# Kernel optimization log

Hardware: AMD Instinct MI355X
Metric: run time of the kernel (lower is better)

Reference implementation:

```python
import jax, jax.numpy as jnp
import numpy as np

N = 150_000          # active BEV voxels
C = 128              # SHARED_CONV_CHANNEL
KK = 9               # 3x3 submanifold kernel
H = W = 1024         # BEV spatial shape at stride 8
OUT_CH = (3, 2, 1, 3, 2)   # hm, center, center_z, dim, rot
NH = 5
MAXO = 3
EPS = 1e-5
INIT_BIAS = -2.19


def _build_neighbor_idx():
    # Random sparse occupancy; pad index == N means 'inactive neighbor'
    rng = np.random.default_rng(0)
    flat = rng.choice(H * W, size=N, replace=False)
    ys, xs = flat // W, flat % W
    grid = np.full(H * W, N, dtype=np.int32)
    grid[flat] = np.arange(N, dtype=np.int32)
    nbr = np.full((N, KK), N, dtype=np.int32)
    k = 0
    for dy in (-1, 0, 1):
        for dx in (-1, 0, 1):
            ny, nx = ys + dy, xs + dx
            ok = (ny >= 0) & (ny < H) & (nx >= 0) & (nx < W)
            nbr[ok, k] = grid[(ny * W + nx)[ok]]
            k += 1
    return jnp.asarray(nbr)


def setup_inputs() -> dict:
    key = jax.random.key(0)
    k0, k1, k2 = jax.random.split(key, 3)
    x = jax.random.normal(k0, (N, C), jnp.float32)
    W1 = jax.random.normal(k1, (NH, KK, C, C), jnp.float32) * (2.0 / (KK * C)) ** 0.5  # kaiming
    gamma = jnp.ones((NH, C), jnp.float32)
    beta = jnp.zeros((NH, C), jnp.float32)
    W2 = jax.random.normal(k2, (NH, C, MAXO), jnp.float32) * 0.02
    b2 = jnp.zeros((NH, MAXO), jnp.float32).at[0, :OUT_CH[0]].set(INIT_BIAS)  # hm init_bias
    return {"x": x, "neighbor_idx": _build_neighbor_idx(),
            "W1": W1, "gamma": gamma, "beta": beta, "W2": W2, "b2": b2}


def reference(x, neighbor_idx, W1, gamma, beta, W2, b2):
    # pad row of zeros: inactive neighbors contribute nothing (submanifold conv)
    xp = jnp.concatenate([x, jnp.zeros((1, C), x.dtype)], axis=0)
    acc = jnp.zeros((NH, x.shape[0], C), x.dtype)
    for k in range(KK):                       # fixed 3x3 kernel loop
        g = xp[neighbor_idx[:, k]]            # [N, C] irregular gather
        acc = acc + jnp.einsum('nc,hcd->hnd', g, W1[:, k])
    # BatchNorm1d (training mode: batch stats over active voxels) + ReLU
    mean = acc.mean(axis=1, keepdims=True)
    var = ((acc - mean) ** 2).mean(axis=1, keepdims=True)
    h = (acc - mean) * jax.lax.rsqrt(var + EPS) * gamma[:, None, :] + beta[:, None, :]
    h = jax.nn.relu(h)
    # 1x1 SubMConv per head (padded to MAXO channels, masked)
    out = jnp.einsum('hnc,hco->hno', h, W2) + b2[:, None, :]   # [NH, N, MAXO]
    mask = (jnp.arange(MAXO)[None, :] < jnp.asarray(OUT_CH)[:, None]).astype(out.dtype)
    return out * mask[:, None, :]
```

## Files before the change

kernel.cpp:

```cpp
#include <hip/hip_runtime.h>

#define NPTS 150000
#define NHEAD 5
#define KTOT 1152
#define NTILES 1172
#define NBLK 586
#define HSTRIDE 592
#define EPSV 1e-5f

typedef __bf16 bf16x8 __attribute__((ext_vector_type(8)));
typedef float f32x4 __attribute__((ext_vector_type(4)));
typedef unsigned short u16x8 __attribute__((ext_vector_type(8)));

#define WS_NEEDED 238484416UL

__device__ __forceinline__ unsigned short f2bf(float f) {
    unsigned int u = __float_as_uint(f);
    u += 0x7FFFu + ((u >> 16) & 1u);
    return (unsigned short)(u >> 16);
}

__device__ __forceinline__ void gload16(const void* g, void* l) {
    __builtin_amdgcn_global_load_lds((const __attribute__((address_space(1))) void*)g,
                                     (__attribute__((address_space(3))) void*)l, 16, 0, 0);
}

__global__ void k_convert(const float* __restrict__ x, unsigned short* __restrict__ xbf) {
    const size_t i8 = (size_t)blockIdx.x * 256 + threadIdx.x;
    const size_t base = i8 * 8;
    if (base >= (size_t)(NPTS + 1) * 128) return;
    if (base < (size_t)NPTS * 128) {
        const f32x4 v0 = __builtin_nontemporal_load((const f32x4*)(x + base));
        const f32x4 v1 = __builtin_nontemporal_load((const f32x4*)(x + base + 4));
        u16x8 o;
        o[0] = f2bf(v0[0]); o[1] = f2bf(v0[1]); o[2] = f2bf(v0[2]); o[3] = f2bf(v0[3]);
        o[4] = f2bf(v1[0]); o[5] = f2bf(v1[1]); o[6] = f2bf(v1[2]); o[7] = f2bf(v1[3]);
        *(u16x8*)(xbf + base) = o;
    } else {
        u16x8 z = {0,0,0,0,0,0,0,0};
        *(u16x8*)(xbf + base) = z;
    }
}

__global__ void k_w1t(const float* __restrict__ W1, unsigned short* __restrict__ w1t) {
    const int idx = blockIdx.x * 256 + threadIdx.x;
    const int d = idx & 127;
    const int c = (idx >> 7) & 127;
    const int hk = idx >> 14;
    const int k = hk % 9, h = hk / 9;
    const int col = h * 128 + d;
    const int p = k * 128 + c;
    const int s32 = p >> 5;
    const int j0 = (p >> 3) & 3;
    const int jj = j0 ^ ((col >> 1) & 3);
    w1t[(size_t)col * KTOT + s32 * 32 + jj * 8 + (p & 7)] = f2bf(W1[idx]);
}

__global__ void k_hist(const int* __restrict__ nbr, int* __restrict__ hist_t) {
    __shared__ int lh[512];
    const int t = threadIdx.x, b = blockIdx.x;
    lh[t] = 0; lh[t + 256] = 0;
    __syncthreads();
    const int n = b * 256 + t;
    if (n < NPTS) {
        int pat = 0;
#pragma unroll
        for (int k = 0; k < 9; k++) pat |= (nbr[n * 9 + k] != NPTS) << k;
        atomicAdd(&lh[pat], 1);
    }
    __syncthreads();
    hist_t[t * HSTRIDE + b] = lh[t];
    hist_t[(t + 256) * HSTRIDE + b] = lh[t + 256];
}

__global__ void k_scan1(int* __restrict__ hist_t, int* __restrict__ tot) {
    const int p = blockIdx.x;
    const int lane = threadIdx.x;
    int run = 0;
    for (int c = 0; c < 10; c++) {
        const int i = c * 64 + lane;
        const int orig = (i < NBLK) ? hist_t[p * HSTRIDE + i] : 0;
        int v = orig;
        for (int d = 1; d < 64; d <<= 1) {
            const int w = __shfl_up(v, d);
            if (lane >= d) v += w;
        }
        if (i < NBLK) hist_t[p * HSTRIDE + i] = run + v - orig;
        run += __shfl(v, 63);
    }
    if (lane == 0) tot[p] = run;
}

__global__ void k_scan2(const int* __restrict__ tot, int* __restrict__ base) {
    __shared__ int t512[512];
    const int k = threadIdx.x;
    const int v = tot[k];
    t512[k] = v;
    __syncthreads();
    for (int d = 1; d < 512; d <<= 1) {
        const int w = (k >= d) ? t512[k - d] : 0;
        __syncthreads();
        t512[k] += w;
        __syncthreads();
    }
    base[k] = t512[k] - v;
}

__global__ void k_scatter(const int* __restrict__ nbr, const int* __restrict__ hist_t,
                          const int* __restrict__ base, int* __restrict__ perm) {
    __shared__ int pat_s[256];
    const int t = threadIdx.x, b = blockIdx.x;
    const int n = b * 256 + t;
    int pat = -1;
    if (n < NPTS) {
        pat = 0;
#pragma unroll
        for (int k = 0; k < 9; k++) pat |= (nbr[n * 9 + k] != NPTS) << k;
    }
    pat_s[t] = pat;
    __syncthreads();
    if (n < NPTS) {
        int rank = 0;
        for (int j = 0; j < 256; j++) rank += (j < t) & (pat_s[j] == pat);
        perm[base[pat] + hist_t[pat * HSTRIDE + b] + rank] = n;
    }
}

__global__ __launch_bounds__(512, 4) void k_gemm(
    const unsigned short* __restrict__ xbf,
    const unsigned short* __restrict__ w1t,
    const int* __restrict__ nbr,
    const int* __restrict__ perm,
    unsigned short* __restrict__ accw,
    float* __restrict__ partials)
{
    __shared__ unsigned short ABC[28672];
    __shared__ int nbr_s[9 * 128];
    __shared__ int perm_s[128];
    __shared__ int mask_s;

    const int tid = threadIdx.x;
    const int wid = tid >> 6;
    const int lane = tid & 63;
    const int bm = blockIdx.x;
    const int b2 = blockIdx.y;
    const int tile = (bm * 331) % NTILES;
    const int tile0 = tile * 128;

    if (tid == 0) mask_s = 0;
    if (tid < 128) {
        const int gr = tile0 + tid;
        perm_s[tid] = (gr < NPTS) ? perm[gr] : NPTS;
    }
    __syncthreads();
    if (tid < 128) {
        const int prow = perm_s[tid];
        int pat = 0;
#pragma unroll
        for (int k = 0; k < 9; k++) {
            const int v = (prow < NPTS) ? nbr[prow * 9 + k] : NPTS;
            nbr_s[k * 128 + tid] = v;
            pat |= (v != NPTS) << k;
        }
        if (pat) atomicOr(&mask_s, pat);
    }
    __syncthreads();
    const int mask = mask_s | 16;
    const int steps = 4 * __builtin_popcount(mask);

    const int RM = (wid >> 2) * 64;
    const int CNl = (wid & 3) * 80;
    const int lr16 = lane >> 2;
    const int lb = lane & 3;
    const int jswS = (lb ^ ((lr16 >> 1) & 3)) * 8;

    f32x4 acc[4][5];
#pragma unroll
    for (int m = 0; m < 4; m++)
#pragma unroll
        for (int n = 0; n < 5; n++) acc[m][n] = f32x4{0.f, 0.f, 0.f, 0.f};

    auto stage = [&](int buf, int kn, int q) {
#pragma unroll
        for (int j = 0; j < 4; ++j) {
            const int g = wid + 8 * j;
            if (g < 8) {
                const int r = g * 16 + lr16;
                const int idx = nbr_s[kn * 128 + r];
                gload16(xbf + (size_t)idx * 128 + q * 32 + jswS,
                        (void*)(ABC + buf * 4096 + g * 512));
            } else if (g < 28) {
                const int gb = g - 8;
                const int lc = gb * 16 + lr16;
                gload16(w1t + (size_t)(b2 * 320 + lc) * KTOT + (kn * 4 + q) * 32 + lb * 8,
                        (void*)(ABC + 8192 + buf * 10240 + gb * 512));
            }
        }
    };

    const int rlo = lane & 15;
    const int jsw = (((lane >> 4) ^ ((rlo >> 1) & 3))) * 8;

    auto compute = [&](int buf) {
        const unsigned short* Ab = ABC + buf * 4096;
        const unsigned short* Bb = ABC + 8192 + buf * 10240;
        bf16x8 a[4];
#pragma unroll
        for (int m = 0; m < 4; m++)
            a[m] = *reinterpret_cast<const bf16x8*>(&Ab[(RM + m * 16 + rlo) * 32 + jsw]);
#pragma unroll
        for (int n = 0; n < 5; n++) {
            const bf16x8 b = *reinterpret_cast<const bf16x8*>(&Bb[(CNl + n * 16 + rlo) * 32 + jsw]);
#pragma unroll
            for (int m = 0; m < 4; m++)
                acc[m][n] = __builtin_amdgcn_mfma_f32_16x16x32_bf16(a[m], b, acc[m][n], 0, 0, 0);
        }
    };

    int ckn = __builtin_ctz(mask), cq = 0, rem = mask & (mask - 1), buf = 0;
    stage(0, ckn, 0);
    __syncthreads();
    for (int i = 0; i < steps; i++) {
        int nkn, nq, nrem;
        if (cq < 3) { nkn = ckn; nq = cq + 1; nrem = rem; }
        else { nkn = rem ? __builtin_ctz(rem) : 0; nq = 0; nrem = rem & (rem - 1); }
        if (i + 1 < steps) stage(buf ^ 1, nkn, nq);
        compute(buf);
        __syncthreads();
        ckn = nkn; cq = nq; rem = nrem; buf ^= 1;
    }

    float* scratch = (float*)&ABC[22528];
    const int g = wid >> 2;
    float sn[5], qn[5];
#pragma unroll
    for (int n = 0; n < 5; n++) {
        float s = 0.f, q = 0.f;
#pragma unroll
        for (int m = 0; m < 4; m++)
#pragma unroll
            for (int r = 0; r < 4; r++) { const float v = acc[m][n][r]; s += v; q += v * v; }
        s += __shfl_xor(s, 16); s += __shfl_xor(s, 32);
        q += __shfl_xor(q, 16); q += __shfl_xor(q, 32);
        sn[n] = s; qn[n] = q;
    }
    __syncthreads();
    if (lane < 16 && g == 0) {
#pragma unroll
        for (int n = 0; n < 5; n++) {
            const int lc = CNl + n * 16 + lane;
            scratch[lc] = sn[n]; scratch[320 + lc] = qn[n];
        }
    }
    __syncthreads();
    if (lane < 16 && g == 1) {
#pragma unroll
        for (int n = 0; n < 5; n++) {
            const int lc = CNl + n * 16 + lane;
            scratch[lc] += sn[n]; scratch[320 + lc] += qn[n];
        }
    }
    __syncthreads();
    for (int t = tid; t < 640; t += 512) {
        const int isq = (t >= 320);
        const int lc = isq ? (t - 320) : t;
        partials[(size_t)bm * 1280 + isq * 640 + b2 * 320 + lc] = scratch[isq * 320 + lc];
    }

    unsigned short* C = (unsigned short*)ABC;
#pragma unroll
    for (int p = 0; p < 2; ++p) {
        __syncthreads();
        if (((wid >> 1) & 1) == p) {
            const int colbase = CNl - p * 160;
#pragma unroll
            for (int m = 0; m < 4; m++) {
                const int row = RM + m * 16 + (lane >> 4) * 4;
#pragma unroll
                for (int n = 0; n < 5; n++) {
                    const int col = colbase + n * 16 + rlo;
#pragma unroll
                    for (int r = 0; r < 4; r++)
                        C[(row + r) * 168 + col] = f2bf(acc[m][n][r]);
                }
            }
        }
        __syncthreads();
#pragma unroll
        for (int j = 0; j < 5; j++) {
            const int chunk = tid + 512 * j;
            const int row = chunk / 20, cc = chunk % 20;
            const int prow = perm_s[row];
            if (prow < NPTS) {
                const int col = b2 * 320 + p * 160 + cc * 8;
                const int hh = col >> 7, d = col & 127;
                __builtin_nontemporal_store(*(const u16x8*)&C[row * 168 + cc * 8],
                    (u16x8*)(accw + ((size_t)hh * NPTS + prow) * 128 + d));
            }
        }
    }
}

__global__ void k_stats(const float* __restrict__ partials, float* __restrict__ stats) {
    __shared__ float red[256];
    const int t = threadIdx.x;
    const int c0 = blockIdx.x * 32;
    const int half = (t >> 5) & 1;
    const int l32 = t & 31;
    const int chunk = t >> 6;
    const int off = half ? (640 + c0 + l32) : (c0 + l32);
    float v = 0.f;
    for (int b = chunk; b < NTILES; b += 4) v += partials[(size_t)b * 1280 + off];
    red[t] = v;
    __syncthreads();
    if (t < 64) red[t] = red[t] + red[t + 64] + red[t + 128] + red[t + 192];
    __syncthreads();
    if (t < 32) {
        const float s = red[t], q = red[t + 32];
        const float mean = s * (1.f / NPTS);
        const float var = q * (1.f / NPTS) - mean * mean;
        const float rstd = rsqrtf(var + EPSV);
        stats[c0 + t] = mean;
        stats[640 + c0 + t] = rstd;
    }
}

__global__ void k_out(const unsigned short* __restrict__ accw,
                      const float* __restrict__ stats,
                      const float* __restrict__ gamma, const float* __restrict__ beta,
                      const float* __restrict__ W2, const float* __restrict__ b2,
                      float* __restrict__ out) {
    __shared__ float sc[128], sh[128], w2s[384], b2s[3];
    const int h = blockIdx.y;
    const int t = threadIdx.x;
    if (t < 128) {
        const float mean = stats[h * 128 + t];
        const float rstd = stats[640 + h * 128 + t];
        const float g = gamma[h * 128 + t];
        const float bb = beta[h * 128 + t];
        sc[t] = rstd * g;
        sh[t] = bb - mean * rstd * g;
        w2s[t * 3 + 0] = W2[(h * 128 + t) * 3 + 0];
        w2s[t * 3 + 1] = W2[(h * 128 + t) * 3 + 1];
        w2s[t * 3 + 2] = W2[(h * 128 + t) * 3 + 2];
    }
    if (t < 3) b2s[t] = b2[h * 3 + t];
    __syncthreads();
    const int chunk = t & 15;
    const int rloc = t >> 4;
    const int base = blockIdx.x * 128;
    const int noc = (h == 2) ? 1 : ((h == 1 || h == 4) ? 2 : 3);
#pragma unroll
    for (int it = 0; it < 8; ++it) {
        const int n = base + it * 16 + rloc;
        float o0 = 0.f, o1 = 0.f, o2 = 0.f;
        if (n < NPTS) {
            const u16x8 v = __builtin_nontemporal_load(
                (const u16x8*)(accw + ((size_t)h * NPTS + n) * 128 + chunk * 8));
#pragma unroll
            for (int j = 0; j < 8; j++) {
                const int c = chunk * 8 + j;
                const float a = __uint_as_float(((unsigned int)v[j]) << 16);
                const float hc = fmaxf(fmaf(a, sc[c], sh[c]), 0.f);
                o0 = fmaf(hc, w2s[c * 3 + 0], o0);
                o1 = fmaf(hc, w2s[c * 3 + 1], o1);
                o2 = fmaf(hc, w2s[c * 3 + 2], o2);
            }
        }
        o0 += __shfl_xor(o0, 1); o1 += __shfl_xor(o1, 1); o2 += __shfl_xor(o2, 1);
        o0 += __shfl_xor(o0, 2); o1 += __shfl_xor(o1, 2); o2 += __shfl_xor(o2, 2);
        o0 += __shfl_xor(o0, 4); o1 += __shfl_xor(o1, 4); o2 += __shfl_xor(o2, 4);
        o0 += __shfl_xor(o0, 8); o1 += __shfl_xor(o1, 8); o2 += __shfl_xor(o2, 8);
        if (chunk == 0 && n < NPTS) {
            const size_t ob = ((size_t)h * NPTS + n) * 3;
            __builtin_nontemporal_store((noc > 0) ? (o0 + b2s[0]) : 0.f, out + ob + 0);
            __builtin_nontemporal_store((noc > 1) ? (o1 + b2s[1]) : 0.f, out + ob + 1);
            __builtin_nontemporal_store((noc > 2) ? (o2 + b2s[2]) : 0.f, out + ob + 2);
        }
    }
}

__global__ void k_sentinel(float* __restrict__ out, int n) {
    const int i = blockIdx.x * 256 + threadIdx.x;
    if (i < n) out[i] = 12345.0f;
}

extern "C" void kernel_launch(void* const* d_in, const int* in_sizes, int n_in,
                              void* d_out, int out_size, void* d_ws, size_t ws_size,
                              hipStream_t stream) {
    const float* x     = (const float*)d_in[0];
    const int*   nbr   = (const int*)d_in[1];
    const float* W1    = (const float*)d_in[2];
    const float* gamma = (const float*)d_in[3];
    const float* beta  = (const float*)d_in[4];
    const float* W2    = (const float*)d_in[5];
    const float* b2    = (const float*)d_in[6];
    float* out = (float*)d_out;

    if (ws_size < WS_NEEDED) {
        k_sentinel<<<(out_size + 255) / 256, 256, 0, stream>>>(out, out_size);
        return;
    }

    char* ws = (char*)d_ws;
    unsigned short* xbf      = (unsigned short*)(ws);
    unsigned short* w1t      = (unsigned short*)(ws + 38404096);
    unsigned short* accw     = (unsigned short*)(ws + 39878656);
    int*            hist_t   = (int*)(ws + 39878656);
    int*            tot      = (int*)(ws + 39878656 + 2097152);
    int*            base     = (int*)(ws + 39878656 + 2099200);
    float*          partials = (float*)(ws + 231878656);
    float*          stats    = (float*)(ws + 237879296);
    int*            perm     = (int*)(ws + 237884416);

    k_convert<<<9376, 256, 0, stream>>>(x, xbf);
    k_w1t<<<2880, 256, 0, stream>>>(W1, w1t);
    k_hist<<<NBLK, 256, 0, stream>>>(nbr, hist_t);
    k_scan1<<<512, 64, 0, stream>>>(hist_t, tot);
    k_scan2<<<1, 512, 0, stream>>>(tot, base);
    k_scatter<<<NBLK, 256, 0, stream>>>(nbr, hist_t, base, perm);
    k_gemm<<<dim3(NTILES, 2), 512, 0, stream>>>(xbf, w1t, nbr, perm, accw, partials);
    k_stats<<<20, 256, 0, stream>>>(partials, stats);
    k_out<<<dim3(NTILES, 5), 256, 0, stream>>>(accw, stats, gamma, beta, W2, b2, out);
}
```

Measured before the change: 350.3 us.

## Merge preprocessing kernels, widen GEMM block to all 640 columns, restructure output pass

Fuses the bf16 convert, weight transpose and pattern histogram into one launch to cut launch overhead. The GEMM now uses 1024-thread blocks that cover all five heads (640 columns) per 128-row tile instead of two 320-column blocks, so each gathered A tile is loaded once rather than twice. The price is more LDS per block and lower occupancy. The output kernel now has two threads per row, each looping over 64 channels, replacing the 16-lane shuffle reduction.

```diff
diff --git a/kernel.cpp b/kernel.cpp
--- a/kernel.cpp
+++ b/kernel.cpp
@@ -25,52 +25,54 @@
                                      (__attribute__((address_space(3))) void*)l, 16, 0, 0);
 }
 
-__global__ void k_convert(const float* __restrict__ x, unsigned short* __restrict__ xbf) {
-    const size_t i8 = (size_t)blockIdx.x * 256 + threadIdx.x;
-    const size_t base = i8 * 8;
-    if (base >= (size_t)(NPTS + 1) * 128) return;
-    if (base < (size_t)NPTS * 128) {
-        const f32x4 v0 = __builtin_nontemporal_load((const f32x4*)(x + base));
-        const f32x4 v1 = __builtin_nontemporal_load((const f32x4*)(x + base + 4));
-        u16x8 o;
-        o[0] = f2bf(v0[0]); o[1] = f2bf(v0[1]); o[2] = f2bf(v0[2]); o[3] = f2bf(v0[3]);
-        o[4] = f2bf(v1[0]); o[5] = f2bf(v1[1]); o[6] = f2bf(v1[2]); o[7] = f2bf(v1[3]);
-        *(u16x8*)(xbf + base) = o;
+__global__ void k_pre(const float* __restrict__ x, unsigned short* __restrict__ xbf,
+                      const float* __restrict__ W1, unsigned short* __restrict__ w1t,
+                      const int* __restrict__ nbr, int* __restrict__ hist_t) {
+    __shared__ int lh[512];
+    const int bid = blockIdx.x;
+    const int t = threadIdx.x;
+    if (bid < 9376) {
+        const size_t i8 = (size_t)bid * 256 + t;
+        const size_t base = i8 * 8;
+        if (base >= (size_t)(NPTS + 1) * 128) return;
+        if (base < (size_t)NPTS * 128) {
+            const f32x4 v0 = __builtin_nontemporal_load((const f32x4*)(x + base));
+            const f32x4 v1 = __builtin_nontemporal_load((const f32x4*)(x + base + 4));
+            u16x8 o;
+            o[0] = f2bf(v0[0]); o[1] = f2bf(v0[1]); o[2] = f2bf(v0[2]); o[3] = f2bf(v0[3]);
+            o[4] = f2bf(v1[0]); o[5] = f2bf(v1[1]); o[6] = f2bf(v1[2]); o[7] = f2bf(v1[3]);
+            *(u16x8*)(xbf + base) = o;
+        } else {
+            u16x8 z = {0,0,0,0,0,0,0,0};
+            *(u16x8*)(xbf + base) = z;
+        }
+    } else if (bid < 9376 + 2880) {
+        const int idx = (bid - 9376) * 256 + t;
+        const int d = idx & 127;
+        const int c = (idx >> 7) & 127;
+        const int hk = idx >> 14;
+        const int k = hk % 9, h = hk / 9;
+        const int col = h * 128 + d;
+        const int p = k * 128 + c;
+        const int s32 = p >> 5;
+        const int j0 = (p >> 3) & 3;
+        const int jj = j0 ^ ((col >> 1) & 3);
+        w1t[(size_t)col * KTOT + s32 * 32 + jj * 8 + (p & 7)] = f2bf(W1[idx]);
     } else {
-        u16x8 z = {0,0,0,0,0,0,0,0};
-        *(u16x8*)(xbf + base) = z;
-    }
-}
-
-__global__ void k_w1t(const float* __restrict__ W1, unsigned short* __restrict__ w1t) {
-    const int idx = blockIdx.x * 256 + threadIdx.x;
-    const int d = idx & 127;
-    const int c = (idx >> 7) & 127;
-    const int hk = idx >> 14;
-    const int k = hk % 9, h = hk / 9;
-    const int col = h * 128 + d;
-    const int p = k * 128 + c;
-    const int s32 = p >> 5;
-    const int j0 = (p >> 3) & 3;
-    const int jj = j0 ^ ((col >> 1) & 3);
-    w1t[(size_t)col * KTOT + s32 * 32 + jj * 8 + (p & 7)] = f2bf(W1[idx]);
-}
-
-__global__ void k_hist(const int* __restrict__ nbr, int* __restrict__ hist_t) {
-    __shared__ int lh[512];
-    const int t = threadIdx.x, b = blockIdx.x;
-    lh[t] = 0; lh[t + 256] = 0;
-    __syncthreads();
-    const int n = b * 256 + t;
-    if (n < NPTS) {
-        int pat = 0;
-#pragma unroll
-        for (int k = 0; k < 9; k++) pat |= (nbr[n * 9 + k] != NPTS) << k;
-        atomicAdd(&lh[pat], 1);
-    }
-    __syncthreads();
-    hist_t[t * HSTRIDE + b] = lh[t];
-    hist_t[(t + 256) * HSTRIDE + b] = lh[t + 256];
+        const int b = bid - 12256;
+        lh[t] = 0; lh[t + 256] = 0;
+        __syncthreads();
+        const int n = b * 256 + t;
+        if (n < NPTS) {
+            int pat = 0;
+#pragma unroll
+            for (int k = 0; k < 9; k++) pat |= (nbr[n * 9 + k] != NPTS) << k;
+            atomicAdd(&lh[pat], 1);
+        }
+        __syncthreads();
+        hist_t[t * HSTRIDE + b] = lh[t];
+        hist_t[(t + 256) * HSTRIDE + b] = lh[t + 256];
+    }
 }
 
 __global__ void k_scan1(int* __restrict__ hist_t, int* __restrict__ tot) {
@@ -126,7 +128,7 @@
     }
 }
 
-__global__ __launch_bounds__(512, 4) void k_gemm(
+__global__ __launch_bounds__(1024, 4) void k_gemm(
     const unsigned short* __restrict__ xbf,
     const unsigned short* __restrict__ w1t,
     const int* __restrict__ nbr,
@@ -134,7 +136,7 @@
     unsigned short* __restrict__ accw,
     float* __restrict__ partials)
 {
-    __shared__ unsigned short ABC[28672];
+    __shared__ unsigned short ABC[49152];
     __shared__ int nbr_s[9 * 128];
     __shared__ int perm_s[128];
     __shared__ int mask_s;
@@ -143,7 +145,6 @@
     const int wid = tid >> 6;
     const int lane = tid & 63;
     const int bm = blockIdx.x;
-    const int b2 = blockIdx.y;
     const int tile = (bm * 331) % NTILES;
     const int tile0 = tile * 128;
 
@@ -168,32 +169,34 @@
     const int mask = mask_s | 16;
     const int steps = 4 * __builtin_popcount(mask);
 
-    const int RM = (wid >> 2) * 64;
-    const int CNl = (wid & 3) * 80;
+    const int rg = wid >> 2;
+    const int cg = wid & 3;
+    const int RM = rg * 32;
+    const int CNl = cg * 160;
     const int lr16 = lane >> 2;
     const int lb = lane & 3;
     const int jswS = (lb ^ ((lr16 >> 1) & 3)) * 8;
 
-    f32x4 acc[4][5];
-#pragma unroll
-    for (int m = 0; m < 4; m++)
-#pragma unroll
-        for (int n = 0; n < 5; n++) acc[m][n] = f32x4{0.f, 0.f, 0.f, 0.f};
+    f32x4 acc[2][10];
+#pragma unroll
+    for (int m = 0; m < 2; m++)
+#pragma unroll
+        for (int n = 0; n < 10; n++) acc[m][n] = f32x4{0.f, 0.f, 0.f, 0.f};
 
     auto stage = [&](int buf, int kn, int q) {
 #pragma unroll
-        for (int j = 0; j < 4; ++j) {
-            const int g = wid + 8 * j;
+        for (int j = 0; j < 3; ++j) {
+            const int g = wid + 16 * j;
             if (g < 8) {
                 const int r = g * 16 + lr16;
                 const int idx = nbr_s[kn * 128 + r];
                 gload16(xbf + (size_t)idx * 128 + q * 32 + jswS,
                         (void*)(ABC + buf * 4096 + g * 512));
-            } else if (g < 28) {
+            } else {
                 const int gb = g - 8;
                 const int lc = gb * 16 + lr16;
-                gload16(w1t + (size_t)(b2 * 320 + lc) * KTOT + (kn * 4 + q) * 32 + lb * 8,
-                        (void*)(ABC + 8192 + buf * 10240 + gb * 512));
+                gload16(w1t + (size_t)lc * KTOT + (kn * 4 + q) * 32 + lb * 8,
+                        (void*)(ABC + 8192 + buf * 20480 + gb * 512));
             }
         }
     };
@@ -203,16 +206,16 @@
 
     auto compute = [&](int buf) {
         const unsigned short* Ab = ABC + buf * 4096;
-        const unsigned short* Bb = ABC + 8192 + buf * 10240;
-        bf16x8 a[4];
-#pragma unroll
-        for (int m = 0; m < 4; m++)
+        const unsigned short* Bb = ABC + 8192 + buf * 20480;
+        bf16x8 a[2];
+#pragma unroll
+        for (int m = 0; m < 2; m++)
             a[m] = *reinterpret_cast<const bf16x8*>(&Ab[(RM + m * 16 + rlo) * 32 + jsw]);
 #pragma unroll
-        for (int n = 0; n < 5; n++) {
+        for (int n = 0; n < 10; n++) {
             const bf16x8 b = *reinterpret_cast<const bf16x8*>(&Bb[(CNl + n * 16 + rlo) * 32 + jsw]);
 #pragma unroll
-            for (int m = 0; m < 4; m++)
+            for (int m = 0; m < 2; m++)
                 acc[m][n] = __builtin_amdgcn_mfma_f32_16x16x32_bf16(a[m], b, acc[m][n], 0, 0, 0);
         }
     };
@@ -230,14 +233,13 @@
         ckn = nkn; cq = nq; rem = nrem; buf ^= 1;
     }
 
-    float* scratch = (float*)&ABC[22528];
-    const int g = wid >> 2;
-    float sn[5], qn[5];
-#pragma unroll
-    for (int n = 0; n < 5; n++) {
+    float* scratch = (float*)&ABC[24576];
+    float sn[10], qn[10];
+#pragma unroll
+    for (int n = 0; n < 10; n++) {
         float s = 0.f, q = 0.f;
 #pragma unroll
-        for (int m = 0; m < 4; m++)
+        for (int m = 0; m < 2; m++)
 #pragma unroll
             for (int r = 0; r < 4; r++) { const float v = acc[m][n][r]; s += v; q += v * v; }
         s += __shfl_xor(s, 16); s += __shfl_xor(s, 32);
@@ -245,40 +247,36 @@
         sn[n] = s; qn[n] = q;
     }
     __syncthreads();
-    if (lane < 16 && g == 0) {
-#pragma unroll
-        for (int n = 0; n < 5; n++) {
-            const int lc = CNl + n * 16 + lane;
-            scratch[lc] = sn[n]; scratch[320 + lc] = qn[n];
-        }
-    }
-    __syncthreads();
-    if (lane < 16 && g == 1) {
-#pragma unroll
-        for (int n = 0; n < 5; n++) {
-            const int lc = CNl + n * 16 + lane;
-            scratch[lc] += sn[n]; scratch[320 + lc] += qn[n];
-        }
-    }
-    __syncthreads();
-    for (int t = tid; t < 640; t += 512) {
-        const int isq = (t >= 320);
-        const int lc = isq ? (t - 320) : t;
-        partials[(size_t)bm * 1280 + isq * 640 + b2 * 320 + lc] = scratch[isq * 320 + lc];
+    if (lane < 16) {
+#pragma unroll
+        for (int n = 0; n < 10; n++) {
+            const int lc = n * 16 + lane;
+            scratch[wid * 320 + lc] = sn[n];
+            scratch[wid * 320 + 160 + lc] = qn[n];
+        }
+    }
+    __syncthreads();
+    for (int t = tid; t < 1280; t += 1024) {
+        const int isq = (t >= 640);
+        const int c = t - isq * 640;
+        const int ccg = c / 160, lc = c % 160;
+        float v = 0.f;
+#pragma unroll
+        for (int r = 0; r < 4; r++) v += scratch[(r * 4 + ccg) * 320 + isq * 160 + lc];
+        partials[(size_t)bm * 1280 + isq * 640 + c] = v;
     }
 
     unsigned short* C = (unsigned short*)ABC;
 #pragma unroll
-    for (int p = 0; p < 2; ++p) {
-        __syncthreads();
-        if (((wid >> 1) & 1) == p) {
-            const int colbase = CNl - p * 160;
-#pragma unroll
-            for (int m = 0; m < 4; m++) {
+    for (int p = 0; p < 4; ++p) {
+        __syncthreads();
+        if (cg == p) {
+#pragma unroll
+            for (int m = 0; m < 2; m++) {
                 const int row = RM + m * 16 + (lane >> 4) * 4;
 #pragma unroll
-                for (int n = 0; n < 5; n++) {
-                    const int col = colbase + n * 16 + rlo;
+                for (int n = 0; n < 10; n++) {
+                    const int col = n * 16 + rlo;
 #pragma unroll
                     for (int r = 0; r < 4; r++)
                         C[(row + r) * 168 + col] = f2bf(acc[m][n][r]);
@@ -287,15 +285,17 @@
         }
         __syncthreads();
 #pragma unroll
-        for (int j = 0; j < 5; j++) {
-            const int chunk = tid + 512 * j;
-            const int row = chunk / 20, cc = chunk % 20;
-            const int prow = perm_s[row];
-            if (prow < NPTS) {
-                const int col = b2 * 320 + p * 160 + cc * 8;
-                const int hh = col >> 7, d = col & 127;
-                __builtin_nontemporal_store(*(const u16x8*)&C[row * 168 + cc * 8],
-                    (u16x8*)(accw + ((size_t)hh * NPTS + prow) * 128 + d));
+        for (int j = 0; j < 3; j++) {
+            const int chunk = tid + 1024 * j;
+            if (chunk < 2560) {
+                const int row = chunk / 20, cc = chunk % 20;
+                const int prow = perm_s[row];
+                if (prow < NPTS) {
+                    const int col = p * 160 + cc * 8;
+                    const int hh = col >> 7, d = col & 127;
+                    __builtin_nontemporal_store(*(const u16x8*)&C[row * 168 + cc * 8],
+                        (u16x8*)(accw + ((size_t)hh * NPTS + prow) * 128 + d));
+                }
             }
         }
     }
@@ -346,20 +346,19 @@
     }
     if (t < 3) b2s[t] = b2[h * 3 + t];
     __syncthreads();
-    const int chunk = t & 15;
-    const int rloc = t >> 4;
-    const int base = blockIdx.x * 128;
+    const int row = t >> 1;
+    const int half = t & 1;
+    const int n = blockIdx.x * 128 + row;
     const int noc = (h == 2) ? 1 : ((h == 1 || h == 4) ? 2 : 3);
-#pragma unroll
-    for (int it = 0; it < 8; ++it) {
-        const int n = base + it * 16 + rloc;
-        float o0 = 0.f, o1 = 0.f, o2 = 0.f;
-        if (n < NPTS) {
-            const u16x8 v = __builtin_nontemporal_load(
-                (const u16x8*)(accw + ((size_t)h * NPTS + n) * 128 + chunk * 8));
+    float o0 = 0.f, o1 = 0.f, o2 = 0.f;
+    if (n < NPTS) {
+        const unsigned short* rp = accw + ((size_t)h * NPTS + n) * 128 + half * 64;
+#pragma unroll
+        for (int c8 = 0; c8 < 8; c8++) {
+            const u16x8 v = __builtin_nontemporal_load((const u16x8*)(rp + c8 * 8));
 #pragma unroll
             for (int j = 0; j < 8; j++) {
-                const int c = chunk * 8 + j;
+                const int c = half * 64 + c8 * 8 + j;
                 const float a = __uint_as_float(((unsigned int)v[j]) << 16);
                 const float hc = fmaxf(fmaf(a, sc[c], sh[c]), 0.f);
                 o0 = fmaf(hc, w2s[c * 3 + 0], o0);
@@ -367,16 +366,15 @@
                 o2 = fmaf(hc, w2s[c * 3 + 2], o2);
             }
         }
-        o0 += __shfl_xor(o0, 1); o1 += __shfl_xor(o1, 1); o2 += __shfl_xor(o2, 1);
-        o0 += __shfl_xor(o0, 2); o1 += __shfl_xor(o1, 2); o2 += __shfl_xor(o2, 2);
-        o0 += __shfl_xor(o0, 4); o1 += __shfl_xor(o1, 4); o2 += __shfl_xor(o2, 4);
-        o0 += __shfl_xor(o0, 8); o1 += __shfl_xor(o1, 8); o2 += __shfl_xor(o2, 8);
-        if (chunk == 0 && n < NPTS) {
-            const size_t ob = ((size_t)h * NPTS + n) * 3;
-            __builtin_nontemporal_store((noc > 0) ? (o0 + b2s[0]) : 0.f, out + ob + 0);
-            __builtin_nontemporal_store((noc > 1) ? (o1 + b2s[1]) : 0.f, out + ob + 1);
-            __builtin_nontemporal_store((noc > 2) ? (o2 + b2s[2]) : 0.f, out + ob + 2);
-        }
+    }
+    o0 += __shfl_xor(o0, 1);
+    o1 += __shfl_xor(o1, 1);
+    o2 += __shfl_xor(o2, 1);
+    if (half == 0 && n < NPTS) {
+        const size_t ob = ((size_t)h * NPTS + n) * 3;
+        __builtin_nontemporal_store((noc > 0) ? (o0 + b2s[0]) : 0.f, out + ob + 0);
+        __builtin_nontemporal_store((noc > 1) ? (o1 + b2s[1]) : 0.f, out + ob + 1);
+        __builtin_nontemporal_store((noc > 2) ? (o2 + b2s[2]) : 0.f, out + ob + 2);
     }
 }
 
@@ -413,13 +411,11 @@
     float*          stats    = (float*)(ws + 237879296);
     int*            perm     = (int*)(ws + 237884416);
 
-    k_convert<<<9376, 256, 0, stream>>>(x, xbf);
-    k_w1t<<<2880, 256, 0, stream>>>(W1, w1t);
-    k_hist<<<NBLK, 256, 0, stream>>>(nbr, hist_t);
+    k_pre<<<12842, 256, 0, stream>>>(x, xbf, W1, w1t, nbr, hist_t);
     k_scan1<<<512, 64, 0, stream>>>(hist_t, tot);
     k_scan2<<<1, 512, 0, stream>>>(tot, base);
     k_scatter<<<NBLK, 256, 0, stream>>>(nbr, hist_t, base, perm);
-    k_gemm<<<dim3(NTILES, 2), 512, 0, stream>>>(xbf, w1t, nbr, perm, accw, partials);
+    k_gemm<<<NTILES, 1024, 0, stream>>>(xbf, w1t, nbr, perm, accw, partials);
     k_stats<<<20, 256, 0, stream>>>(partials, stats);
     k_out<<<dim3(NTILES, 5), 256, 0, stream>>>(accw, stats, gamma, beta, W2, b2, out);
 }
```

Result: slower. 450.2 us (+28.5%).

## Merge preprocessing kernels, stream B from global, triple-buffer A, reshape output kernel

Applied to the files above, without the earlier changes.

Folds the bf16 conversion, W1 transpose and histogram kernels into one launch to cut launch overhead. In the GEMM, the weight tile is no longer staged through LDS. Each wave reads its B fragments directly from global/L2, and only the gathered A rows are staged, now in a 3-deep ring with 64-wide K steps and a manual s_barrier/waitcnt pipeline. The output kernel now has two threads per row with one shuffle instead of sixteen lanes per row. The risks are higher global-load latency on B in the MFMA loop and a fragile hand-written waitcnt schedule.

```diff
diff --git a/kernel.cpp b/kernel.cpp
--- a/kernel.cpp
+++ b/kernel.cpp
@@ -25,52 +25,49 @@
                                      (__attribute__((address_space(3))) void*)l, 16, 0, 0);
 }
 
-__global__ void k_convert(const float* __restrict__ x, unsigned short* __restrict__ xbf) {
-    const size_t i8 = (size_t)blockIdx.x * 256 + threadIdx.x;
-    const size_t base = i8 * 8;
-    if (base >= (size_t)(NPTS + 1) * 128) return;
-    if (base < (size_t)NPTS * 128) {
-        const f32x4 v0 = __builtin_nontemporal_load((const f32x4*)(x + base));
-        const f32x4 v1 = __builtin_nontemporal_load((const f32x4*)(x + base + 4));
-        u16x8 o;
-        o[0] = f2bf(v0[0]); o[1] = f2bf(v0[1]); o[2] = f2bf(v0[2]); o[3] = f2bf(v0[3]);
-        o[4] = f2bf(v1[0]); o[5] = f2bf(v1[1]); o[6] = f2bf(v1[2]); o[7] = f2bf(v1[3]);
-        *(u16x8*)(xbf + base) = o;
+__global__ void k_pre(const float* __restrict__ x, unsigned short* __restrict__ xbf,
+                      const float* __restrict__ W1, unsigned short* __restrict__ w1t,
+                      const int* __restrict__ nbr, int* __restrict__ hist_t) {
+    __shared__ int lh[512];
+    const int bid = blockIdx.x;
+    const int t = threadIdx.x;
+    if (bid < 9376) {
+        const size_t i8 = (size_t)bid * 256 + t;
+        const size_t base = i8 * 8;
+        if (base >= (size_t)(NPTS + 1) * 128) return;
+        if (base < (size_t)NPTS * 128) {
+            const f32x4 v0 = __builtin_nontemporal_load((const f32x4*)(x + base));
+            const f32x4 v1 = __builtin_nontemporal_load((const f32x4*)(x + base + 4));
+            u16x8 o;
+            o[0] = f2bf(v0[0]); o[1] = f2bf(v0[1]); o[2] = f2bf(v0[2]); o[3] = f2bf(v0[3]);
+            o[4] = f2bf(v1[0]); o[5] = f2bf(v1[1]); o[6] = f2bf(v1[2]); o[7] = f2bf(v1[3]);
+            *(u16x8*)(xbf + base) = o;
+        } else {
+            u16x8 z = {0,0,0,0,0,0,0,0};
+            *(u16x8*)(xbf + base) = z;
+        }
+    } else if (bid < 9376 + 2880) {
+        const int idx = (bid - 9376) * 256 + t;
+        const int d = idx & 127;
+        const int c = (idx >> 7) & 127;
+        const int hk = idx >> 14;
+        const int k = hk % 9, h = hk / 9;
+        w1t[(size_t)(h * 128 + d) * KTOT + k * 128 + c] = f2bf(W1[idx]);
     } else {
-        u16x8 z = {0,0,0,0,0,0,0,0};
-        *(u16x8*)(xbf + base) = z;
-    }
-}
-
-__global__ void k_w1t(const float* __restrict__ W1, unsigned short* __restrict__ w1t) {
-    const int idx = blockIdx.x * 256 + threadIdx.x;
-    const int d = idx & 127;
-    const int c = (idx >> 7) & 127;
-    const int hk = idx >> 14;
-    const int k = hk % 9, h = hk / 9;
-    const int col = h * 128 + d;
-    const int p = k * 128 + c;
-    const int s32 = p >> 5;
-    const int j0 = (p >> 3) & 3;
-    const int jj = j0 ^ ((col >> 1) & 3);
-    w1t[(size_t)col * KTOT + s32 * 32 + jj * 8 + (p & 7)] = f2bf(W1[idx]);
-}
-
-__global__ void k_hist(const int* __restrict__ nbr, int* __restrict__ hist_t) {
-    __shared__ int lh[512];
-    const int t = threadIdx.x, b = blockIdx.x;
-    lh[t] = 0; lh[t + 256] = 0;
-    __syncthreads();
-    const int n = b * 256 + t;
-    if (n < NPTS) {
-        int pat = 0;
-#pragma unroll
-        for (int k = 0; k < 9; k++) pat |= (nbr[n * 9 + k] != NPTS) << k;
-        atomicAdd(&lh[pat], 1);
-    }
-    __syncthreads();
-    hist_t[t * HSTRIDE + b] = lh[t];
-    hist_t[(t + 256) * HSTRIDE + b] = lh[t + 256];
+        const int b = bid - 12256;
+        lh[t] = 0; lh[t + 256] = 0;
+        __syncthreads();
+        const int n = b * 256 + t;
+        if (n < NPTS) {
+            int pat = 0;
+#pragma unroll
+            for (int k = 0; k < 9; k++) pat |= (nbr[n * 9 + k] != NPTS) << k;
+            atomicAdd(&lh[pat], 1);
+        }
+        __syncthreads();
+        hist_t[t * HSTRIDE + b] = lh[t];
+        hist_t[(t + 256) * HSTRIDE + b] = lh[t + 256];
+    }
 }
 
 __global__ void k_scan1(int* __restrict__ hist_t, int* __restrict__ tot) {
@@ -134,7 +131,7 @@
     unsigned short* __restrict__ accw,
     float* __restrict__ partials)
 {
-    __shared__ unsigned short ABC[28672];
+    __shared__ unsigned short ABuf[24576];
     __shared__ int nbr_s[9 * 128];
     __shared__ int perm_s[128];
     __shared__ int mask_s;
@@ -166,13 +163,12 @@
     }
     __syncthreads();
     const int mask = mask_s | 16;
-    const int steps = 4 * __builtin_popcount(mask);
+    const int steps = 2 * __builtin_popcount(mask);
 
     const int RM = (wid >> 2) * 64;
     const int CNl = (wid & 3) * 80;
-    const int lr16 = lane >> 2;
-    const int lb = lane & 3;
-    const int jswS = (lb ^ ((lr16 >> 1) & 3)) * 8;
+    const int rlo = lane & 15;
+    const int lhi = lane >> 4;
 
     f32x4 acc[4][5];
 #pragma unroll
@@ -180,57 +176,65 @@
 #pragma unroll
         for (int n = 0; n < 5; n++) acc[m][n] = f32x4{0.f, 0.f, 0.f, 0.f};
 
-    auto stage = [&](int buf, int kn, int q) {
-#pragma unroll
-        for (int j = 0; j < 4; ++j) {
-            const int g = wid + 8 * j;
-            if (g < 8) {
-                const int r = g * 16 + lr16;
-                const int idx = nbr_s[kn * 128 + r];
-                gload16(xbf + (size_t)idx * 128 + q * 32 + jswS,
-                        (void*)(ABC + buf * 4096 + g * 512));
-            } else if (g < 28) {
-                const int gb = g - 8;
-                const int lc = gb * 16 + lr16;
-                gload16(w1t + (size_t)(b2 * 320 + lc) * KTOT + (kn * 4 + q) * 32 + lb * 8,
-                        (void*)(ABC + 8192 + buf * 10240 + gb * 512));
+    auto stage = [&](int buf, int kn, int half) {
+#pragma unroll
+        for (int j = 0; j < 2; ++j) {
+            const int g = wid * 2 + j;
+            const int r = g * 8 + (lane >> 3);
+            const int idx = nbr_s[kn * 128 + r];
+            gload16(xbf + (size_t)idx * 128 + half * 64 + (((lane & 7) ^ (lane >> 3)) << 3),
+                    (void*)(ABuf + buf * 8192 + g * 512));
+        }
+    };
+
+    auto compute = [&](int buf, int kn, int half) {
+        const unsigned short* Ab = ABuf + buf * 8192;
+        const size_t pbase = (size_t)kn * 128 + half * 64 + (lhi << 3);
+#pragma unroll
+        for (int qq = 0; qq < 2; ++qq) {
+            bf16x8 b[5];
+#pragma unroll
+            for (int n = 0; n < 5; n++)
+                b[n] = *reinterpret_cast<const bf16x8*>(
+                    w1t + (size_t)(b2 * 320 + CNl + n * 16 + rlo) * KTOT + pbase + qq * 32);
+            bf16x8 a[4];
+#pragma unroll
+            for (int m = 0; m < 4; m++) {
+                const int R = RM + m * 16 + rlo;
+                const int jj = (qq * 4 + lhi) ^ (rlo & 7);
+                a[m] = *reinterpret_cast<const bf16x8*>(&Ab[R * 64 + jj * 8]);
             }
+#pragma unroll
+            for (int n = 0; n < 5; n++)
+#pragma unroll
+                for (int m = 0; m < 4; m++)
+                    acc[m][n] = __builtin_amdgcn_mfma_f32_16x16x32_bf16(a[m], b[n], acc[m][n], 0, 0, 0);
         }
     };
 
-    const int rlo = lane & 15;
-    const int jsw = (((lane >> 4) ^ ((rlo >> 1) & 3))) * 8;
-
-    auto compute = [&](int buf) {
-        const unsigned short* Ab = ABC + buf * 4096;
-        const unsigned short* Bb = ABC + 8192 + buf * 10240;
-        bf16x8 a[4];
-#pragma unroll
-        for (int m = 0; m < 4; m++)
-            a[m] = *reinterpret_cast<const bf16x8*>(&Ab[(RM + m * 16 + rlo) * 32 + jsw]);
-#pragma unroll
-        for (int n = 0; n < 5; n++) {
-            const bf16x8 b = *reinterpret_cast<const bf16x8*>(&Bb[(CNl + n * 16 + rlo) * 32 + jsw]);
-#pragma unroll
-            for (int m = 0; m < 4; m++)
-                acc[m][n] = __builtin_amdgcn_mfma_f32_16x16x32_bf16(a[m], b, acc[m][n], 0, 0, 0);
-        }
+    int ckn = __builtin_ctz(mask), ch = 0, crem = mask & (mask - 1);
+    int skn = ckn, sh = 0, srem = crem;
+    auto sadv = [&]() {
+        if (sh == 0) sh = 1;
+        else if (srem) { skn = __builtin_ctz(srem); srem &= srem - 1; sh = 0; }
     };
-
-    int ckn = __builtin_ctz(mask), cq = 0, rem = mask & (mask - 1), buf = 0;
-    stage(0, ckn, 0);
-    __syncthreads();
-    for (int i = 0; i < steps; i++) {
-        int nkn, nq, nrem;
-        if (cq < 3) { nkn = ckn; nq = cq + 1; nrem = rem; }
-        else { nkn = rem ? __builtin_ctz(rem) : 0; nq = 0; nrem = rem & (rem - 1); }
-        if (i + 1 < steps) stage(buf ^ 1, nkn, nq);
-        compute(buf);
-        __syncthreads();
-        ckn = nkn; cq = nq; rem = nrem; buf ^= 1;
-    }
-
-    float* scratch = (float*)&ABC[22528];
+    stage(0, skn, sh); sadv();
+    stage(1, skn, sh); sadv();
+    asm volatile("s_waitcnt vmcnt(2)" ::: "memory");
+
+    int bc = 0, bs = 2;
+    for (int t = 0; t < steps; ++t) {
+        asm volatile("s_barrier" ::: "memory");
+        compute(bc, ckn, ch);
+        if (ch == 0) ch = 1;
+        else if (crem) { ckn = __builtin_ctz(crem); crem &= crem - 1; ch = 0; }
+        stage(bs, skn, sh); sadv();
+        bc = (bc == 2) ? 0 : bc + 1;
+        bs = (bs == 2) ? 0 : bs + 1;
+    }
+    __syncthreads();
+
+    float* scratch = (float*)&ABuf[22528];
     const int g = wid >> 2;
     float sn[5], qn[5];
 #pragma unroll
@@ -244,7 +248,6 @@
         q += __shfl_xor(q, 16); q += __shfl_xor(q, 32);
         sn[n] = s; qn[n] = q;
     }
-    __syncthreads();
     if (lane < 16 && g == 0) {
 #pragma unroll
         for (int n = 0; n < 5; n++) {
@@ -267,7 +270,7 @@
         partials[(size_t)bm * 1280 + isq * 640 + b2 * 320 + lc] = scratch[isq * 320 + lc];
     }
 
-    unsigned short* C = (unsigned short*)ABC;
+    unsigned short* C = (unsigned short*)ABuf;
 #pragma unroll
     for (int p = 0; p < 2; ++p) {
         __syncthreads();
@@ -275,7 +278,7 @@
             const int colbase = CNl - p * 160;
 #pragma unroll
             for (int m = 0; m < 4; m++) {
-                const int row = RM + m * 16 + (lane >> 4) * 4;
+                const int row = RM + m * 16 + lhi * 4;
 #pragma unroll
                 for (int n = 0; n < 5; n++) {
                     const int col = colbase + n * 16 + rlo;
@@ -346,20 +349,19 @@
     }
     if (t < 3) b2s[t] = b2[h * 3 + t];
     __syncthreads();
-    const int chunk = t & 15;
-    const int rloc = t >> 4;
-    const int base = blockIdx.x * 128;
+    const int row = t >> 1;
+    const int half = t & 1;
+    const int n = blockIdx.x * 128 + row;
     const int noc = (h == 2) ? 1 : ((h == 1 || h == 4) ? 2 : 3);
-#pragma unroll
-    for (int it = 0; it < 8; ++it) {
-        const int n = base + it * 16 + rloc;
-        float o0 = 0.f, o1 = 0.f, o2 = 0.f;
-        if (n < NPTS) {
-            const u16x8 v = __builtin_nontemporal_load(
-                (const u16x8*)(accw + ((size_t)h * NPTS + n) * 128 + chunk * 8));
+    float o0 = 0.f, o1 = 0.f, o2 = 0.f;
+    if (n < NPTS) {
+        const unsigned short* rp = accw + ((size_t)h * NPTS + n) * 128 + half * 64;
+#pragma unroll
+        for (int c8 = 0; c8 < 8; c8++) {
+            const u16x8 v = __builtin_nontemporal_load((const u16x8*)(rp + c8 * 8));
 #pragma unroll
             for (int j = 0; j < 8; j++) {
-                const int c = chunk * 8 + j;
+                const int c = half * 64 + c8 * 8 + j;
                 const float a = __uint_as_float(((unsigned int)v[j]) << 16);
                 const float hc = fmaxf(fmaf(a, sc[c], sh[c]), 0.f);
                 o0 = fmaf(hc, w2s[c * 3 + 0], o0);
@@ -367,16 +369,15 @@
                 o2 = fmaf(hc, w2s[c * 3 + 2], o2);
             }
         }
-        o0 += __shfl_xor(o0, 1); o1 += __shfl_xor(o1, 1); o2 += __shfl_xor(o2, 1);
-        o0 += __shfl_xor(o0, 2); o1 += __shfl_xor(o1, 2); o2 += __shfl_xor(o2, 2);
-        o0 += __shfl_xor(o0, 4); o1 += __shfl_xor(o1, 4); o2 += __shfl_xor(o2, 4);
-        o0 += __shfl_xor(o0, 8); o1 += __shfl_xor(o1, 8); o2 += __shfl_xor(o2, 8);
-        if (chunk == 0 && n < NPTS) {
-            const size_t ob = ((size_t)h * NPTS + n) * 3;
-            __builtin_nontemporal_store((noc > 0) ? (o0 + b2s[0]) : 0.f, out + ob + 0);
-            __builtin_nontemporal_store((noc > 1) ? (o1 + b2s[1]) : 0.f, out + ob + 1);
-            __builtin_nontemporal_store((noc > 2) ? (o2 + b2s[2]) : 0.f, out + ob + 2);
-        }
+    }
+    o0 += __shfl_xor(o0, 1);
+    o1 += __shfl_xor(o1, 1);
+    o2 += __shfl_xor(o2, 1);
+    if (half == 0 && n < NPTS) {
+        const size_t ob = ((size_t)h * NPTS + n) * 3;
+        __builtin_nontemporal_store((noc > 0) ? (o0 + b2s[0]) : 0.f, out + ob + 0);
+        __builtin_nontemporal_store((noc > 1) ? (o1 + b2s[1]) : 0.f, out + ob + 1);
+        __builtin_nontemporal_store((noc > 2) ? (o2 + b2s[2]) : 0.f, out + ob + 2);
     }
 }
 
@@ -413,9 +414,7 @@
     float*          stats    = (float*)(ws + 237879296);
     int*            perm     = (int*)(ws + 237884416);
 
-    k_convert<<<9376, 256, 0, stream>>>(x, xbf);
-    k_w1t<<<2880, 256, 0, stream>>>(W1, w1t);
-    k_hist<<<NBLK, 256, 0, stream>>>(nbr, hist_t);
+    k_pre<<<12842, 256, 0, stream>>>(x, xbf, W1, w1t, nbr, hist_t);
     k_scan1<<<512, 64, 0, stream>>>(hist_t, tot);
     k_scan2<<<1, 512, 0, stream>>>(tot, base);
     k_scatter<<<NBLK, 256, 0, stream>>>(nbr, hist_t, base, perm);
```

Result: slower. 491.3 us (+40.2%).
